# Kernel tuning notes

Hardware: AMD Instinct MI355X
Metric: run time of the kernel (lower is better)

## Reference

```python
import jax, jax.numpy as jnp
import numpy as np

H, W = 512, 512
N = 10240
CHUNK = 128  # gaussians per scan step; peak intermediate CHUNK*H*W floats
ALPHA_MIN = 1.0 / 255.0
ALPHA_MAX = 0.999


def setup_inputs() -> dict:
    key = jax.random.key(0)
    k1, k2, k3, k4 = jax.random.split(key, 4)
    # matches torch init: _xyz = atanh(2*(rand-0.5)); others = rand
    u = jax.random.uniform(k1, (N, 2), dtype=jnp.float32)
    xyz = jnp.arctanh(jnp.clip(2.0 * (u - 0.5), -0.999, 0.999))
    cholesky = jax.random.uniform(k2, (N, 3), dtype=jnp.float32)
    opacity = jax.random.uniform(k3, (N, 1), dtype=jnp.float32)
    features = jax.random.uniform(k4, (N, 3), dtype=jnp.float32)
    return {"xyz": xyz, "cholesky": cholesky, "opacity": opacity, "features": features}


def _render(xyz, cholesky, opacity, features):
    # project_gaussians_2d: mean in [-1,1] via tanh -> pixel coords
    mean = jnp.tanh(xyz)                      # [N,2]
    cx = 0.5 * W * (mean[:, 0] + 1.0)         # [N]
    cy = 0.5 * H * (mean[:, 1] + 1.0)
    # cholesky_bound = [0.5, 0, 0.5]
    l = cholesky + jnp.array([0.5, 0.0, 0.5], dtype=cholesky.dtype)
    l1, l2, l3 = l[:, 0], l[:, 1], l[:, 2]
    # cov = L L^T with L = [[l1,0],[l2,l3]]
    c00 = l1 * l1
    c01 = l1 * l2
    c11 = l2 * l2 + l3 * l3
    det = c00 * c11 - c01 * c01               # = (l1*l3)^2
    inv = 1.0 / det
    A = c11 * inv                             # conic.x
    B = -c01 * inv                            # conic.y
    C = c00 * inv                             # conic.z
    opac = opacity[:, 0]

    xs = jnp.arange(W, dtype=mean.dtype) + 0.5  # pixel centers
    ys = jnp.arange(H, dtype=mean.dtype) + 0.5

    nch = N // CHUNK

    def resh(t):
        return t.reshape(nch, CHUNK, *t.shape[1:])

    scan_args = (resh(cx), resh(cy), resh(A), resh(B), resh(C), resh(opac), resh(features))

    def body(img, a):
        cx_, cy_, A_, B_, C_, op_, col_ = a
        dx = cx_[:, None] - xs[None, :]       # [CHUNK, W]
        dy = cy_[:, None] - ys[None, :]       # [CHUNK, H]
        # sigma = 0.5*(A dx^2 + C dy^2) + B dx dy  (per gaussian, per pixel)
        sigma = (0.5 * A_[:, None, None] * (dx * dx)[:, None, :]
                 + 0.5 * C_[:, None, None] * (dy * dy)[:, :, None]
                 + B_[:, None, None] * dy[:, :, None] * dx[:, None, :])  # [CHUNK,H,W]
        alpha = jnp.minimum(ALPHA_MAX, op_[:, None, None] * jnp.exp(-sigma))
        alpha = jnp.where((sigma >= 0.0) & (alpha >= ALPHA_MIN), alpha, 0.0)
        img = img + jnp.einsum('nhw,nc->hwc', alpha, col_)
        return img, None

    img0 = jnp.zeros((H, W, 3), dtype=mean.dtype)
    img, _ = jax.lax.scan(body, img0, scan_args)
    img = jnp.clip(img, 0.0, 1.0)
    # view(-1,H,W,3).permute(0,3,1,2)
    return img.reshape(1, H, W, 3).transpose(0, 3, 1, 2)


def reference(xyz, cholesky, opacity, features):
    return _render(xyz, cholesky, opacity, features)
```

## Files before the change

### kernel.cpp

```cpp
#include <hip/hip_runtime.h>
#include <math.h>

#define HH 512
#define WW 512
#define NN 10240
#define A_MIN (1.0f/255.0f)
#define A_MAX 0.999f

#define RB 16
#define WAVES 16
#define WRANGE (NN/WAVES)
#define WCHUNKS (WRANGE/64)
#define RCAP 24
#define RSLOTS (WAVES*RCAP)
#define PCAP 128

__global__ __launch_bounds__(256) void prep_kernel(
    const float* __restrict__ xyz, const float* __restrict__ chol,
    const float* __restrict__ opac, const float* __restrict__ feat,
    float4* __restrict__ P0, float4* __restrict__ P1,
    float* __restrict__ P2b, unsigned int* __restrict__ Qt) {
  int n = blockIdx.x * 256 + threadIdx.x;
  if (n >= NN) return;
  float mx = tanhf(xyz[2*n+0]);
  float my = tanhf(xyz[2*n+1]);
  float cx = 0.5f * WW * (mx + 1.0f);
  float cy = 0.5f * HH * (my + 1.0f);
  float l1 = chol[3*n+0] + 0.5f;
  float l2 = chol[3*n+1];
  float l3 = chol[3*n+2] + 0.5f;
  float c00 = l1*l1;
  float c01 = l1*l2;
  float c11 = l2*l2 + l3*l3;
  float det = c00*c11 - c01*c01;
  float inv = 1.0f / det;
  float A = c11 * inv;
  float B = -c01 * inv;
  float C = c00 * inv;
  float op = opac[n];
  P0[n]  = make_float4(cx, cy, 0.5f * A, B);
  P1[n]  = make_float4(0.5f * C, op, feat[3*n+0], feat[3*n+1]);
  P2b[n] = feat[3*n+2];

  unsigned int q = 0x000000FFu;
  float smax = logf(op * 255.0f);
  if (smax > 0.0f) {
    float rx = sqrtf(2.0f * smax * c00) + 1.0f;
    float ry = sqrtf(2.0f * smax * c11) + 1.0f;
    int px0 = max(0,    (int)floorf(cx - rx));
    int px1 = min(WW-1, (int)floorf(cx + rx));
    int py0 = max(0,    (int)floorf(cy - ry));
    int py1 = min(HH-1, (int)floorf(cy + ry));
    if (px0 <= px1 && py0 <= py1) {
      unsigned int tx0 = px0 >> 4, tx1 = px1 >> 4;
      unsigned int ty0 = py0 >> 4, ty1 = py1 >> 4;
      q = tx0 | (tx1 << 8) | (ty0 << 16) | (ty1 << 24);
    }
  }
  Qt[n] = q;
}

__global__ __launch_bounds__(1024, 4) void render_kernel(
    const float4* __restrict__ P0, const float4* __restrict__ P1,
    const float* __restrict__ P2b, const unsigned int* __restrict__ Qt,
    float* __restrict__ out)
{
  __shared__ uint2          reg2[RSLOTS];
  __shared__ int            rcnt[WAVES];
  __shared__ unsigned short qseg[4][PCAP];
  __shared__ int            qcnt[4];
  __shared__ float4         pA[4][PCAP];
  __shared__ float4         pB[4][PCAP];
  __shared__ float          pC[4][PCAP];

  const int tid  = threadIdx.x;
  const int bx   = blockIdx.x, by = blockIdx.y;
  const int w    = tid >> 6;
  const int lane = tid & 63;

  {
    const int tx0r = 2*bx, tx1r = 2*bx + 1;
    const int ty0r = 2*by, ty1r = 2*by + 1;
    int base = 0;
    for (int c = 0; c < WCHUNKS; ++c) {
      int n = w*WRANGE + c*64 + lane;
      unsigned int v = Qt[n];
      int gtx0 = v & 0xFF, gtx1 = (v >> 8) & 0xFF;
      int gty0 = (v >> 16) & 0xFF, gty1 = v >> 24;
      bool hit = (gtx0 <= tx1r) & (gtx1 >= tx0r) & (gty0 <= ty1r) & (gty1 >= ty0r);
      unsigned long long m = __ballot(hit);
      int idx = base + (int)__popcll(m & ((1ull << lane) - 1ull));
      if (hit && idx < RCAP) reg2[w*RCAP + idx] = make_uint2(v, (unsigned)n);
      base += (int)__popcll(m);
      if (base >= RCAP) { base = RCAP; break; }
    }
    if (lane == 0) rcnt[w] = base;
  }
  __syncthreads();

  if (w < 4) {
    const int q   = w;
    const int ttx = 2*bx + (q & 1);
    const int tty = 2*by + (q >> 1);
    int base = 0;
    for (int c = 0; c < RSLOTS/64; ++c) {
      int slot = c*64 + lane;
      int rr = slot / RCAP;
      int j  = slot - rr*RCAP;
      bool valid = j < rcnt[rr];
      unsigned int v = 0x000000FFu, n = 0;
      if (valid) { uint2 e = reg2[slot]; v = e.x; n = e.y; }
      int gtx0 = v & 0xFF, gtx1 = (v >> 8) & 0xFF;
      int gty0 = (v >> 16) & 0xFF, gty1 = v >> 24;
      bool hit = valid & (gtx0 <= ttx) & (gtx1 >= ttx) & (gty0 <= tty) & (gty1 >= tty);
      unsigned long long m = __ballot(hit);
      int idx = base + (int)__popcll(m & ((1ull << lane) - 1ull));
      if (hit && idx < PCAP) qseg[q][idx] = (unsigned short)n;
      base += (int)__popcll(m);
    }
    if (lane == 0) qcnt[q] = min(base, PCAP);
  }
  __syncthreads();

  {
    int q = tid >> 8;
    int s = tid & 255;
    if (s < qcnt[q]) {
      int n = qseg[q][s];
      pA[q][s] = P0[n];
      pB[q][s] = P1[n];
      pC[q][s] = P2b[n];
    }
  }
  __syncthreads();

  {
    int q = tid >> 8;
    int s = tid & 255;
    int lx = s & 15, ly = s >> 4;
    int x = bx*32 + (q & 1)*16 + lx;
    int y = by*32 + (q >> 1)*16 + ly;
    float px = x + 0.5f, py = y + 0.5f;
    int tot = qcnt[q];
    float accR = 0.0f, accG = 0.0f, accB = 0.0f;
    for (int j = 0; j < tot; ++j) {
      float4 pa = pA[q][j];
      float4 pb = pB[q][j];
      float dx = pa.x - px;
      float dy = pa.y - py;
      float sigma = pa.z*dx*dx + pb.x*dy*dy + pa.w*dy*dx;
      float alpha = fminf(A_MAX, pb.y * __expf(-sigma));
      if (sigma >= 0.0f && alpha >= A_MIN) {
        accR += alpha * pb.z;
        accG += alpha * pb.w;
        accB += alpha * pC[q][j];
      }
    }
    int pix = y * WW + x;
    out[pix]              = fminf(fmaxf(accR, 0.0f), 1.0f);
    out[HH*WW + pix]      = fminf(fmaxf(accG, 0.0f), 1.0f);
    out[2*HH*WW + pix]    = fminf(fmaxf(accB, 0.0f), 1.0f);
  }
}

extern "C" void kernel_launch(void* const* d_in, const int* in_sizes, int n_in,
                              void* d_out, int out_size, void* d_ws, size_t ws_size,
                              hipStream_t stream) {
  const float* xyz  = (const float*)d_in[0];
  const float* chol = (const float*)d_in[1];
  const float* opac = (const float*)d_in[2];
  const float* feat = (const float*)d_in[3];

  char* ws = (char*)d_ws;
  float4*       P0  = (float4*)(ws);
  float4*       P1  = (float4*)(ws + (size_t)NN * 16);
  float*        P2b = (float*) (ws + (size_t)NN * 32);
  unsigned int* Qt  = (unsigned int*)(ws + (size_t)NN * 36);

  prep_kernel<<<(NN + 255) / 256, 256, 0, stream>>>(xyz, chol, opac, feat, P0, P1, P2b, Qt);
  render_kernel<<<dim3(RB, RB), 1024, 0, stream>>>(P0, P1, P2b, Qt, (float*)d_out);
}
```

Baseline: 22.00 us.

## Fuse gaussian preprocessing into render kernel with conservative per-block culling

Drops the separate prep kernel and its global workspace. Each render block now tests every gaussian against its 32x32 region itself, computing the centre with a fast exp-based tanh and a conservative radius taken from an upper bound on opacity. Only the surviving candidates get full conic and tile-bounds setup, written straight into shared memory, and the per-quadrant lists then index those shared slots. This removes one launch and a global write/read round trip, at the cost of every block redundantly reading xyz and cholesky for all gaussians and doing transcendental work on them.

```diff
diff --git a/kernel.cpp b/kernel.cpp
--- a/kernel.cpp
+++ b/kernel.cpp
@@ -14,64 +14,21 @@
 #define RCAP 24
 #define RSLOTS (WAVES*RCAP)
 #define PCAP 128
+#define SMAX_UB 5.5452f
 
-__global__ __launch_bounds__(256) void prep_kernel(
+__global__ __launch_bounds__(1024) void fused_kernel(
     const float* __restrict__ xyz, const float* __restrict__ chol,
     const float* __restrict__ opac, const float* __restrict__ feat,
-    float4* __restrict__ P0, float4* __restrict__ P1,
-    float* __restrict__ P2b, unsigned int* __restrict__ Qt) {
-  int n = blockIdx.x * 256 + threadIdx.x;
-  if (n >= NN) return;
-  float mx = tanhf(xyz[2*n+0]);
-  float my = tanhf(xyz[2*n+1]);
-  float cx = 0.5f * WW * (mx + 1.0f);
-  float cy = 0.5f * HH * (my + 1.0f);
-  float l1 = chol[3*n+0] + 0.5f;
-  float l2 = chol[3*n+1];
-  float l3 = chol[3*n+2] + 0.5f;
-  float c00 = l1*l1;
-  float c01 = l1*l2;
-  float c11 = l2*l2 + l3*l3;
-  float det = c00*c11 - c01*c01;
-  float inv = 1.0f / det;
-  float A = c11 * inv;
-  float B = -c01 * inv;
-  float C = c00 * inv;
-  float op = opac[n];
-  P0[n]  = make_float4(cx, cy, 0.5f * A, B);
-  P1[n]  = make_float4(0.5f * C, op, feat[3*n+0], feat[3*n+1]);
-  P2b[n] = feat[3*n+2];
-
-  unsigned int q = 0x000000FFu;
-  float smax = logf(op * 255.0f);
-  if (smax > 0.0f) {
-    float rx = sqrtf(2.0f * smax * c00) + 1.0f;
-    float ry = sqrtf(2.0f * smax * c11) + 1.0f;
-    int px0 = max(0,    (int)floorf(cx - rx));
-    int px1 = min(WW-1, (int)floorf(cx + rx));
-    int py0 = max(0,    (int)floorf(cy - ry));
-    int py1 = min(HH-1, (int)floorf(cy + ry));
-    if (px0 <= px1 && py0 <= py1) {
-      unsigned int tx0 = px0 >> 4, tx1 = px1 >> 4;
-      unsigned int ty0 = py0 >> 4, ty1 = py1 >> 4;
-      q = tx0 | (tx1 << 8) | (ty0 << 16) | (ty1 << 24);
-    }
-  }
-  Qt[n] = q;
-}
-
-__global__ __launch_bounds__(1024, 4) void render_kernel(
-    const float4* __restrict__ P0, const float4* __restrict__ P1,
-    const float* __restrict__ P2b, const unsigned int* __restrict__ Qt,
     float* __restrict__ out)
 {
-  __shared__ uint2          reg2[RSLOTS];
-  __shared__ int            rcnt[WAVES];
-  __shared__ unsigned short qseg[4][PCAP];
-  __shared__ int            qcnt[4];
-  __shared__ float4         pA[4][PCAP];
-  __shared__ float4         pB[4][PCAP];
-  __shared__ float          pC[4][PCAP];
+  __shared__ int          ridx[RSLOTS];
+  __shared__ int          rcnt[WAVES];
+  __shared__ float4       pA[RSLOTS];
+  __shared__ float4       pB[RSLOTS];
+  __shared__ float        pC[RSLOTS];
+  __shared__ unsigned int qw[RSLOTS];
+  __shared__ short        qseg[4][PCAP];
+  __shared__ int          qcnt[4];
 
   const int tid  = threadIdx.x;
   const int bx   = blockIdx.x, by = blockIdx.y;
@@ -79,22 +36,79 @@
   const int lane = tid & 63;
 
   {
-    const int tx0r = 2*bx, tx1r = 2*bx + 1;
-    const int ty0r = 2*by, ty1r = 2*by + 1;
+    const float rx0 = 32.f * bx,  rx1 = 32.f * bx + 32.f;
+    const float ry0 = 32.f * by,  ry1 = 32.f * by + 32.f;
     int base = 0;
     for (int c = 0; c < WCHUNKS; ++c) {
-      int n = w*WRANGE + c*64 + lane;
-      unsigned int v = Qt[n];
-      int gtx0 = v & 0xFF, gtx1 = (v >> 8) & 0xFF;
-      int gty0 = (v >> 16) & 0xFF, gty1 = v >> 24;
-      bool hit = (gtx0 <= tx1r) & (gtx1 >= tx0r) & (gty0 <= ty1r) & (gty1 >= ty0r);
+      int n = w * WRANGE + c * 64 + lane;
+      float2 xy = ((const float2*)xyz)[n];
+      float l1 = chol[3*n+0] + 0.5f;
+      float l2 = chol[3*n+1];
+      float l3 = chol[3*n+2] + 0.5f;
+      float c00 = l1*l1;
+      float c11 = l2*l2 + l3*l3;
+      float ex = __expf(2.f * xy.x);
+      float ey = __expf(2.f * xy.y);
+      float cx = 256.f * (2.f - __fdividef(2.f, ex + 1.f));
+      float cy = 256.f * (2.f - __fdividef(2.f, ey + 1.f));
+      float rx2 = 2.f * SMAX_UB * c00;
+      float ry2 = 2.f * SMAX_UB * c11;
+      float gx = fmaxf(fmaxf(rx0 - cx, cx - rx1), 0.f) - 1.1f;
+      float gy = fmaxf(fmaxf(ry0 - cy, cy - ry1), 0.f) - 1.1f;
+      gx = fmaxf(gx, 0.f);
+      gy = fmaxf(gy, 0.f);
+      bool hit = (gx * gx <= rx2) & (gy * gy <= ry2);
       unsigned long long m = __ballot(hit);
       int idx = base + (int)__popcll(m & ((1ull << lane) - 1ull));
-      if (hit && idx < RCAP) reg2[w*RCAP + idx] = make_uint2(v, (unsigned)n);
+      if (hit && idx < RCAP) ridx[w * RCAP + idx] = n;
       base += (int)__popcll(m);
       if (base >= RCAP) { base = RCAP; break; }
     }
     if (lane == 0) rcnt[w] = base;
+  }
+  __syncthreads();
+
+  if (tid < RSLOTS) {
+    int rr = tid / RCAP;
+    int j  = tid - rr * RCAP;
+    unsigned int q = 0x000000FFu;
+    if (j < rcnt[rr]) {
+      int n = ridx[tid];
+      float mx = tanhf(xyz[2*n+0]);
+      float my = tanhf(xyz[2*n+1]);
+      float cx = 0.5f * WW * (mx + 1.0f);
+      float cy = 0.5f * HH * (my + 1.0f);
+      float l1 = chol[3*n+0] + 0.5f;
+      float l2 = chol[3*n+1];
+      float l3 = chol[3*n+2] + 0.5f;
+      float c00 = l1*l1;
+      float c01 = l1*l2;
+      float c11 = l2*l2 + l3*l3;
+      float det = c00*c11 - c01*c01;
+      float inv = 1.0f / det;
+      float A = c11 * inv;
+      float B = -c01 * inv;
+      float C = c00 * inv;
+      float op = opac[n];
+      pA[tid] = make_float4(cx, cy, 0.5f * A, B);
+      pB[tid] = make_float4(0.5f * C, op, feat[3*n+0], feat[3*n+1]);
+      pC[tid] = feat[3*n+2];
+      float smax = logf(op * 255.0f);
+      if (smax > 0.0f) {
+        float rx = sqrtf(2.0f * smax * c00) + 1.0f;
+        float ry = sqrtf(2.0f * smax * c11) + 1.0f;
+        int px0 = max(0,    (int)floorf(cx - rx));
+        int px1 = min(WW-1, (int)floorf(cx + rx));
+        int py0 = max(0,    (int)floorf(cy - ry));
+        int py1 = min(HH-1, (int)floorf(cy + ry));
+        if (px0 <= px1 && py0 <= py1) {
+          unsigned int tx0 = px0 >> 4, tx1 = px1 >> 4;
+          unsigned int ty0 = py0 >> 4, ty1 = py1 >> 4;
+          q = tx0 | (tx1 << 8) | (ty0 << 16) | (ty1 << 24);
+        }
+      }
+    }
+    qw[tid] = q;
   }
   __syncthreads();
 
@@ -105,32 +119,16 @@
     int base = 0;
     for (int c = 0; c < RSLOTS/64; ++c) {
       int slot = c*64 + lane;
-      int rr = slot / RCAP;
-      int j  = slot - rr*RCAP;
-      bool valid = j < rcnt[rr];
-      unsigned int v = 0x000000FFu, n = 0;
-      if (valid) { uint2 e = reg2[slot]; v = e.x; n = e.y; }
-      int gtx0 = v & 0xFF, gtx1 = (v >> 8) & 0xFF;
-      int gty0 = (v >> 16) & 0xFF, gty1 = v >> 24;
-      bool hit = valid & (gtx0 <= ttx) & (gtx1 >= ttx) & (gty0 <= tty) & (gty1 >= tty);
+      unsigned int v = qw[slot];
+      int tx0 = v & 0xFF, tx1 = (v >> 8) & 0xFF;
+      int ty0 = (v >> 16) & 0xFF, ty1 = v >> 24;
+      bool hit = (tx0 <= ttx) & (tx1 >= ttx) & (ty0 <= tty) & (ty1 >= tty);
       unsigned long long m = __ballot(hit);
       int idx = base + (int)__popcll(m & ((1ull << lane) - 1ull));
-      if (hit && idx < PCAP) qseg[q][idx] = (unsigned short)n;
+      if (hit && idx < PCAP) qseg[q][idx] = (short)slot;
       base += (int)__popcll(m);
     }
     if (lane == 0) qcnt[q] = min(base, PCAP);
-  }
-  __syncthreads();
-
-  {
-    int q = tid >> 8;
-    int s = tid & 255;
-    if (s < qcnt[q]) {
-      int n = qseg[q][s];
-      pA[q][s] = P0[n];
-      pB[q][s] = P1[n];
-      pC[q][s] = P2b[n];
-    }
   }
   __syncthreads();
 
@@ -144,8 +142,9 @@
     int tot = qcnt[q];
     float accR = 0.0f, accG = 0.0f, accB = 0.0f;
     for (int j = 0; j < tot; ++j) {
-      float4 pa = pA[q][j];
-      float4 pb = pB[q][j];
+      int slot = qseg[q][j];
+      float4 pa = pA[slot];
+      float4 pb = pB[slot];
       float dx = pa.x - px;
       float dy = pa.y - py;
       float sigma = pa.z*dx*dx + pb.x*dy*dy + pa.w*dy*dx;
@@ -153,13 +152,13 @@
       if (sigma >= 0.0f && alpha >= A_MIN) {
         accR += alpha * pb.z;
         accG += alpha * pb.w;
-        accB += alpha * pC[q][j];
+        accB += alpha * pC[slot];
       }
     }
     int pix = y * WW + x;
-    out[pix]              = fminf(fmaxf(accR, 0.0f), 1.0f);
-    out[HH*WW + pix]      = fminf(fmaxf(accG, 0.0f), 1.0f);
-    out[2*HH*WW + pix]    = fminf(fmaxf(accB, 0.0f), 1.0f);
+    out[pix]           = fminf(fmaxf(accR, 0.0f), 1.0f);
+    out[HH*WW + pix]   = fminf(fmaxf(accG, 0.0f), 1.0f);
+    out[2*HH*WW + pix] = fminf(fmaxf(accB, 0.0f), 1.0f);
   }
 }
 
@@ -171,12 +170,5 @@
   const float* opac = (const float*)d_in[2];
   const float* feat = (const float*)d_in[3];
 
-  char* ws = (char*)d_ws;
-  float4*       P0  = (float4*)(ws);
-  float4*       P1  = (float4*)(ws + (size_t)NN * 16);
-  float*        P2b = (float*) (ws + (size_t)NN * 32);
-  unsigned int* Qt  = (unsigned int*)(ws + (size_t)NN * 36);
-
-  prep_kernel<<<(NN + 255) / 256, 256, 0, stream>>>(xyz, chol, opac, feat, P0, P1, P2b, Qt);
-  render_kernel<<<dim3(RB, RB), 1024, 0, stream>>>(P0, P1, P2b, Qt, (float*)d_out);
+  fused_kernel<<<dim3(RB, RB), 1024, 0, stream>>>(xyz, chol, opac, feat, (float*)d_out);
 }
```

After: 19.75 us. 1.11x faster.
